# Optimization experiments

Hardware: AMD Instinct MI355X
Metric: run time of the kernel (lower is better)

## Reference

```python
import jax, jax.numpy as jnp
import numpy as np

NUM_NODE = 50000
HIDDEN = 64
GAMMA = 0.01
ITERS = 5
INIT_SCALE = 0.1  # ~ xavier std for 64x64, keeps exp(sigmoid/gamma) finite in fp32


def setup_inputs() -> dict:
    key = jax.random.key(0)
    M = jax.random.normal(key, (NUM_NODE, HIDDEN, HIDDEN), dtype=jnp.float32) * INIT_SCALE
    return {"M": M}


def reference(M):
    # C = exp(sigmoid(clamp(M)) / gamma), per-node (H, H) matrix
    M1 = jnp.clip(M, -10.0, 10.0)
    C = jnp.exp(jax.nn.sigmoid(M1) / GAMMA)
    for _ in range(ITERS):
        # norm1(C.T).T : column-normalize (sum over rows, axis=1 of each HxH block)
        C = C / C.sum(axis=1, keepdims=True)
        # norm1(C)     : row-normalize (sum over cols, axis=2 of each HxH block)
        C = C / C.sum(axis=2, keepdims=True)
    return C
```

## Files before the change

### kernel.cpp

```cpp
#include <hip/hip_runtime.h>


#define LOG2E 1.4426950408889634f

__device__ __forceinline__ float fast_rcp(float x) {
    return __builtin_amdgcn_rcpf(x);
}
__device__ __forceinline__ float fast_exp2(float x) {
    return __builtin_amdgcn_exp2f(x);
}

__global__ __launch_bounds__(256) void sinkhorn_kernel(
    const float* __restrict__ M, float* __restrict__ out, int num_node) {

    const int wavesPerBlock = blockDim.x >> 6;
    const int node = blockIdx.x * wavesPerBlock + (threadIdx.x >> 6);
    if (node >= num_node) return;
    const int lane = threadIdx.x & 63;

    const float* __restrict__ Mn = M + (size_t)node * 4096;
    float* __restrict__ On = out + (size_t)node * 4096;

    float c[16][4];
    #pragma unroll
    for (int t = 0; t < 16; ++t) {
        const float4 val = *reinterpret_cast<const float4*>(Mn + 256 * t + 4 * lane);
        c[t][0] = val.x; c[t][1] = val.y; c[t][2] = val.z; c[t][3] = val.w;
    }

    #pragma unroll
    for (int t = 0; t < 16; ++t) {
        #pragma unroll
        for (int k = 0; k < 4; ++k) {
            float x = c[t][k];
            x = fminf(10.0f, fmaxf(-10.0f, x));
            float e = fast_exp2(-x * LOG2E);
            float s = fast_rcp(1.0f + e);
            c[t][k] = fast_exp2(s * (100.0f * LOG2E));
        }
    }

    float u[16];
    #pragma unroll
    for (int t = 0; t < 16; ++t) u[t] = 1.0f;
    float v[4] = {1.0f, 1.0f, 1.0f, 1.0f};

    #pragma unroll
    for (int it = 0; it < 5; ++it) {
        float d[4];
        #pragma unroll
        for (int k = 0; k < 4; ++k) {
            float acc = 0.0f;
            #pragma unroll
            for (int t = 0; t < 16; ++t) acc = fmaf(u[t], c[t][k], acc);
            d[k] = acc;
        }
        #pragma unroll
        for (int k = 0; k < 4; ++k) {
            d[k] += __shfl_xor(d[k], 16, 64);
            d[k] += __shfl_xor(d[k], 32, 64);
            v[k] = fast_rcp(d[k]);
        }
        #pragma unroll
        for (int t = 0; t < 16; ++t) {
            float acc = 0.0f;
            #pragma unroll
            for (int k = 0; k < 4; ++k) acc = fmaf(c[t][k], v[k], acc);
            acc += __shfl_xor(acc, 1, 64);
            acc += __shfl_xor(acc, 2, 64);
            acc += __shfl_xor(acc, 4, 64);
            acc += __shfl_xor(acc, 8, 64);
            u[t] = fast_rcp(acc);
        }
    }

    #pragma unroll
    for (int t = 0; t < 16; ++t) {
        float4 o;
        o.x = u[t] * c[t][0] * v[0];
        o.y = u[t] * c[t][1] * v[1];
        o.z = u[t] * c[t][2] * v[2];
        o.w = u[t] * c[t][3] * v[3];
        *reinterpret_cast<float4*>(On + 256 * t + 4 * lane) = o;
    }
}

extern "C" void kernel_launch(void* const* d_in, const int* in_sizes, int n_in,
                              void* d_out, int out_size, void* d_ws, size_t ws_size,
                              hipStream_t stream) {
    const float* M = (const float*)d_in[0];
    float* out = (float*)d_out;
    const int num_node = in_sizes[0] / 4096;

    const int wavesPerBlock = 4;
    const int blocks = (num_node + wavesPerBlock - 1) / wavesPerBlock;
    sinkhorn_kernel<<<blocks, 256, 0, stream>>>(M, out, num_node);
}
```

Baseline: 325.3 us.

## Split each node's sinkhorn across four waves with LDS column-sum exchange

Each 64x64 node matrix is now handled by a 256-thread block instead of a single wave. Each wave owns 16 rows, column partial sums are combined through a double-buffered shared-memory exchange with a block barrier, and row sums stay wave-local via shuffles. This cuts per-thread register use from 64 matrix values to 16 and raises occupancy to hide memory latency. In exchange it adds a barrier and LDS traffic on every iteration.

```diff
diff --git a/kernel.cpp b/kernel.cpp
--- a/kernel.cpp
+++ b/kernel.cpp
@@ -10,26 +10,30 @@
     return __builtin_amdgcn_exp2f(x);
 }
 
-__global__ __launch_bounds__(256) void sinkhorn_kernel(
+__global__ __launch_bounds__(256, 8) void sinkhorn_kernel(
     const float* __restrict__ M, float* __restrict__ out, int num_node) {
 
-    const int wavesPerBlock = blockDim.x >> 6;
-    const int node = blockIdx.x * wavesPerBlock + (threadIdx.x >> 6);
+    __shared__ float xch[2][4][64];
+
+    const int node = blockIdx.x;
     if (node >= num_node) return;
-    const int lane = threadIdx.x & 63;
+    const int tid  = threadIdx.x;
+    const int w    = tid >> 6;
+    const int lane = tid & 63;
+    const int cg   = lane & 15;
 
-    const float* __restrict__ Mn = M + (size_t)node * 4096;
-    float* __restrict__ On = out + (size_t)node * 4096;
+    const float* __restrict__ Mn = M + (size_t)node * 4096 + 1024 * w;
+    float* __restrict__ On = out + (size_t)node * 4096 + 1024 * w;
 
-    float c[16][4];
+    float c[4][4];
     #pragma unroll
-    for (int t = 0; t < 16; ++t) {
+    for (int t = 0; t < 4; ++t) {
         const float4 val = *reinterpret_cast<const float4*>(Mn + 256 * t + 4 * lane);
         c[t][0] = val.x; c[t][1] = val.y; c[t][2] = val.z; c[t][3] = val.w;
     }
 
     #pragma unroll
-    for (int t = 0; t < 16; ++t) {
+    for (int t = 0; t < 4; ++t) {
         #pragma unroll
         for (int k = 0; k < 4; ++k) {
             float x = c[t][k];
@@ -40,42 +44,55 @@
         }
     }
 
-    float u[16];
-    #pragma unroll
-    for (int t = 0; t < 16; ++t) u[t] = 1.0f;
+    float u[4] = {1.0f, 1.0f, 1.0f, 1.0f};
     float v[4] = {1.0f, 1.0f, 1.0f, 1.0f};
 
     #pragma unroll
     for (int it = 0; it < 5; ++it) {
-        float d[4];
+        const int buf = it & 1;
+
+        float pd[4];
         #pragma unroll
         for (int k = 0; k < 4; ++k) {
-            float acc = 0.0f;
+            float a = 0.0f;
             #pragma unroll
-            for (int t = 0; t < 16; ++t) acc = fmaf(u[t], c[t][k], acc);
-            d[k] = acc;
+            for (int t = 0; t < 4; ++t) a = fmaf(u[t], c[t][k], a);
+            a += __shfl_xor(a, 16, 64);
+            a += __shfl_xor(a, 32, 64);
+            pd[k] = a;
         }
+        if (lane < 16) {
+            *reinterpret_cast<float4*>(&xch[buf][w][4 * cg]) =
+                make_float4(pd[0], pd[1], pd[2], pd[3]);
+        }
+        __syncthreads();
+
+        {
+            const float4 s0 = *reinterpret_cast<const float4*>(&xch[buf][0][4 * cg]);
+            const float4 s1 = *reinterpret_cast<const float4*>(&xch[buf][1][4 * cg]);
+            const float4 s2 = *reinterpret_cast<const float4*>(&xch[buf][2][4 * cg]);
+            const float4 s3 = *reinterpret_cast<const float4*>(&xch[buf][3][4 * cg]);
+            v[0] = fast_rcp(s0.x + s1.x + s2.x + s3.x);
+            v[1] = fast_rcp(s0.y + s1.y + s2.y + s3.y);
+            v[2] = fast_rcp(s0.z + s1.z + s2.z + s3.z);
+            v[3] = fast_rcp(s0.w + s1.w + s2.w + s3.w);
+        }
+
         #pragma unroll
-        for (int k = 0; k < 4; ++k) {
-            d[k] += __shfl_xor(d[k], 16, 64);
-            d[k] += __shfl_xor(d[k], 32, 64);
-            v[k] = fast_rcp(d[k]);
-        }
-        #pragma unroll
-        for (int t = 0; t < 16; ++t) {
-            float acc = 0.0f;
+        for (int t = 0; t < 4; ++t) {
+            float a = 0.0f;
             #pragma unroll
-            for (int k = 0; k < 4; ++k) acc = fmaf(c[t][k], v[k], acc);
-            acc += __shfl_xor(acc, 1, 64);
-            acc += __shfl_xor(acc, 2, 64);
-            acc += __shfl_xor(acc, 4, 64);
-            acc += __shfl_xor(acc, 8, 64);
-            u[t] = fast_rcp(acc);
+            for (int k = 0; k < 4; ++k) a = fmaf(c[t][k], v[k], a);
+            a += __shfl_xor(a, 1, 64);
+            a += __shfl_xor(a, 2, 64);
+            a += __shfl_xor(a, 4, 64);
+            a += __shfl_xor(a, 8, 64);
+            u[t] = fast_rcp(a);
         }
     }
 
     #pragma unroll
-    for (int t = 0; t < 16; ++t) {
+    for (int t = 0; t < 4; ++t) {
         float4 o;
         o.x = u[t] * c[t][0] * v[0];
         o.y = u[t] * c[t][1] * v[1];
@@ -92,7 +109,5 @@
     float* out = (float*)d_out;
     const int num_node = in_sizes[0] / 4096;
 
-    const int wavesPerBlock = 4;
-    const int blocks = (num_node + wavesPerBlock - 1) / wavesPerBlock;
-    sinkhorn_kernel<<<blocks, 256, 0, stream>>>(M, out, num_node);
+    sinkhorn_kernel<<<num_node, 256, 0, stream>>>(M, out, num_node);
 }
```

Result: slower. 347.8 us (+6.9%).
